# Optimization experiments

Hardware: AMD Instinct MI355X
Metric: run time of the kernel (lower is better)

## Reference

```python
import jax, jax.numpy as jnp
import numpy as np

B, X, Y, Z, T = 2, 32, 32, 32, 16
WIDTH = 20
M1, M2, M3, M4 = 8, 8, 8, 6
N_LAYERS = 8  # octant count per spectral layer


def spectral_conv4d(x, w_ri, m1, m2, m3, m4):
    """x: [B, Ci, X, Y, Z, T] real. w_ri: [8, Ci, Co, m1, m2, m3, m4, 2] real/imag."""
    w = w_ri[..., 0] + 1j * w_ri[..., 1]  # [8, Ci, Co, m1, m2, m3, m4] complex64
    b, ci = x.shape[0], x.shape[1]
    xs, ys, zs, ts = x.shape[2], x.shape[3], x.shape[4], x.shape[5]
    co = w.shape[2]
    # fftn followed by keeping last-dim modes [:m4] equals rfftn at those bins
    x_ft = jnp.fft.rfftn(x, axes=(-4, -3, -2, -1))  # [B, Ci, X, Y, Z, T//2+1]
    out_ft = jnp.zeros((b, co, xs, ys, zs, ts // 2 + 1), dtype=x_ft.dtype)
    idx = 0
    for s1 in (slice(0, m1), slice(xs - m1, xs)):
        for s2 in (slice(0, m2), slice(ys - m2, ys)):
            for s3 in (slice(0, m3), slice(zs - m3, zs)):
                blk = jnp.einsum('bixyzt,ioxyzt->boxyzt',
                                 x_ft[:, :, s1, s2, s3, :m4], w[idx])
                out_ft = out_ft.at[:, :, s1, s2, s3, :m4].set(blk)
                idx += 1
    return jnp.fft.irfftn(out_ft, s=(xs, ys, zs, ts), axes=(-4, -3, -2, -1))


def gelu(x):
    return jax.nn.gelu(x, approximate=False)  # matches torch F.gelu (erf)


def setup_inputs() -> dict:
    key = jax.random.key(0)
    ks = jax.random.split(key, 10)
    scale = 1.0 / (WIDTH * WIDTH)
    return {
        'x': jax.random.normal(ks[0], (B, X, Y, Z, T, 5), dtype=jnp.float32),
        'fc0_w': jax.random.normal(ks[1], (5, WIDTH), dtype=jnp.float32) * 0.3,
        'fc0_b': jax.random.normal(ks[2], (WIDTH,), dtype=jnp.float32) * 0.1,
        'sw': jax.random.uniform(ks[3], (4, 8, WIDTH, WIDTH, M1, M2, M3, M4, 2),
                                 dtype=jnp.float32) * scale,
        'ww': jax.random.normal(ks[4], (4, WIDTH, WIDTH), dtype=jnp.float32) * 0.15,
        'wb': jax.random.normal(ks[5], (4, WIDTH), dtype=jnp.float32) * 0.1,
        'fc1_w': jax.random.normal(ks[6], (WIDTH, 128), dtype=jnp.float32) * 0.15,
        'fc1_b': jax.random.normal(ks[7], (128,), dtype=jnp.float32) * 0.1,
        'fc2_w': jax.random.normal(ks[8], (128, 1), dtype=jnp.float32) * 0.1,
        'fc2_b': jax.random.normal(ks[9], (1,), dtype=jnp.float32) * 0.1,
    }


def reference(x, fc0_w, fc0_b, sw, ww, wb, fc1_w, fc1_b, fc2_w, fc2_b):
    # Lift: [B, X, Y, Z, T, 5] -> [B, X, Y, Z, T, W] -> channels-first
    h = jnp.einsum('bxyzti,iw->bxyztw', x, fc0_w) + fc0_b
    h = jnp.transpose(h, (0, 5, 1, 2, 3, 4))  # [B, W, X, Y, Z, T]
    for l in range(4):
        h1 = spectral_conv4d(h, sw[l], M1, M2, M3, M4)
        h2 = jnp.einsum('bixyzt,oi->boxyzt', h, ww[l]) \
             + wb[l][None, :, None, None, None, None]
        h = h1 + h2
        if l < 3:
            h = gelu(h)  # dropout is identity at inference
    h = jnp.transpose(h, (0, 2, 3, 4, 5, 1))  # [B, X, Y, Z, T, W]
    h = gelu(jnp.einsum('bxyztw,wh->bxyzth', h, fc1_w) + fc1_b)
    out = jnp.einsum('bxyzth,ho->bxyzto', h, fc2_w) + fc2_b
    return out
```

## Files before the change

kernel.cpp:

```cpp
#include <hip/hip_runtime.h>

typedef float2 cplx;

#define SPAT 524288
#define TWO_PI_16 0.39269908169872414f
#define TWO_PI_32 0.19634954084936207f

#define H_OFF   0u
#define A_OFF   83886080u
#define BT_OFF  (83886080u + 31457280u)
#define CT_OFF  (83886080u + 31457280u + 7864320u)
#define FLAG_OFF (83886080u + 31457280u + 7864320u + 7864320u)
#define WS_NEED (FLAG_OFF + 64u)

__device__ __forceinline__ float bf2f(unsigned short s){
    union { unsigned int u; float f; } v; v.u = ((unsigned int)s) << 16; return v.f;
}
__device__ __forceinline__ unsigned short f2bf(float f){
    union { float ff; unsigned int u; } v; v.ff = f;
    unsigned int u = v.u;
    u += 0x7fffu + ((u >> 16) & 1u);
    return (unsigned short)(u >> 16);
}
__device__ __forceinline__ cplx bf2c(unsigned int p){
    union { unsigned int u; float f; } a, b;
    a.u = p << 16; b.u = p & 0xffff0000u;
    cplx r; r.x = a.f; r.y = b.f; return r;
}
__device__ __forceinline__ float LDR(const void* p, size_t i, int bf){
    return bf ? bf2f(((const unsigned short*)p)[i]) : ((const float*)p)[i];
}
__device__ __forceinline__ void STR(void* p, size_t i, float v, int bf){
    if (bf) ((unsigned short*)p)[i] = f2bf(v);
    else    ((float*)p)[i] = v;
}
__device__ __forceinline__ void cmadd(cplx& d, const cplx a, const cplx b){
    d.x = fmaf(a.x, b.x, d.x);
    d.x = fmaf(-a.y, b.y, d.x);
    d.y = fmaf(a.x, b.y, d.y);
    d.y = fmaf(a.y, b.x, d.y);
}
__device__ __forceinline__ int freqm(int m){ return m + ((m >> 3) << 4); }
__device__ __forceinline__ float gelu_f(float v){
    return 0.5f * v * (1.0f + erff(v * 0.7071067811865475f));
}

__global__ void k_detect(const unsigned short* __restrict__ x, int* __restrict__ flag){
    __shared__ int cnts[64];
    const int tid = threadIdx.x;
    int cnt = 0;
    for (int j = tid; j < 512; j += 64){
        unsigned short u = x[2 * j];
        unsigned int e = (u >> 7) & 0xFFu;
        if (e < 27u || e > 160u) cnt++;
    }
    cnts[tid] = cnt;
    __syncthreads();
    if (tid == 0){
        int s = 0;
        for (int i = 0; i < 64; i++) s += cnts[i];
        flag[0] = (s > 64) ? 0 : 1;
    }
}

__global__ __launch_bounds__(256) void k_fc0(const int* __restrict__ flag,
                                             const void* __restrict__ x,
                                             const void* __restrict__ w,
                                             const void* __restrict__ bias,
                                             float* __restrict__ h){
    const int bf = flag[0];
    __shared__ float sw[100];
    __shared__ float sb[20];
    const int tid = threadIdx.x;
    if (tid < 100) sw[tid] = LDR(w, tid, bf);
    if (tid < 20)  sb[tid] = LDR(bias, tid, bf);
    __syncthreads();
    const int p = blockIdx.x * 256 + tid;
    const int b = p >> 19;
    const int rem = p & (SPAT - 1);
    float xi[5];
    #pragma unroll
    for (int i = 0; i < 5; i++) xi[i] = LDR(x, (size_t)p * 5 + i, bf);
    const size_t ob = (size_t)b * 20 * SPAT + rem;
    #pragma unroll
    for (int c = 0; c < 20; c++){
        float acc = sb[c];
        #pragma unroll
        for (int i = 0; i < 5; i++) acc = fmaf(xi[i], sw[i * 20 + c], acc);
        h[ob + (size_t)c * SPAT] = acc;
    }
}

__global__ __launch_bounds__(512, 4) void k_fwdTZY(const float* __restrict__ h, cplx* __restrict__ A2){
    const int x  = blockIdx.x;
    const int bc = blockIdx.y;
    __shared__ __align__(16) float buf[12356];
    __shared__ cplx w16[16];
    __shared__ cplx twZ[16][33];
    const int tid = threadIdx.x;
    if (tid < 16){
        float s, c; sincosf(-TWO_PI_16 * (float)tid, &s, &c);
        w16[tid] = make_float2(c, s);
    }
    if (tid < 512){
        int m = tid >> 5, z = tid & 31;
        float s, c; sincosf(-TWO_PI_32 * (float)((freqm(m) * z) & 31), &s, &c);
        twZ[m][z] = make_float2(c, s);
    }
    __syncthreads();
    cplx wreg[16];
    #pragma unroll
    for (int j = 0; j < 16; j++) wreg[j] = w16[j];
    const float* src = h + ((size_t)bc * 1024 + x * 32) * 512;
    #pragma unroll
    for (int r = 0; r < 2; r++){
        int l = tid + (r << 9);
        int zz = l & 31, y = l >> 5;
        const float4* g = (const float4*)(src + (size_t)y * 512 + zz * 16);
        float4 q0 = g[0], q1 = g[1], q2 = g[2], q3 = g[3];
        float v[16] = {q0.x,q0.y,q0.z,q0.w, q1.x,q1.y,q1.z,q1.w,
                       q2.x,q2.y,q2.z,q2.w, q3.x,q3.y,q3.z,q3.w};
        const int W = y * 386 + zz * 12 + 2 * (zz >> 3);
        float s0 = 0.f;
        #pragma unroll
        for (int t = 0; t < 16; t++) s0 += v[t];
        *(cplx*)&buf[W] = make_float2(s0, 0.f);
        #pragma unroll
        for (int k = 1; k < 6; k++){
            float ax = 0.f, ay = 0.f;
            #pragma unroll
            for (int t = 0; t < 16; t++){
                cplx w = wreg[(k * t) & 15];
                ax = fmaf(v[t], w.x, ax);
                ay = fmaf(v[t], w.y, ay);
            }
            *(cplx*)&buf[W + 2 * k] = make_float2(ax, ay);
        }
    }
    __syncthreads();
    cplx acc2[6];
    #pragma unroll
    for (int r = 0; r < 6; r++){
        int idx = tid + (r << 9);
        int y = idx & 31, q = idx >> 5;
        int k = q % 6, mz = q / 6;
        cplx a = make_float2(0.f, 0.f);
        #pragma unroll
        for (int zz = 0; zz < 32; zz++){
            cplx vz = *(const cplx*)&buf[y * 386 + zz * 12 + 2 * (zz >> 3) + 2 * k];
            cmadd(a, vz, twZ[mz][zz]);
        }
        acc2[r] = a;
    }
    __syncthreads();
    #pragma unroll
    for (int r = 0; r < 6; r++){
        int idx = tid + (r << 9);
        int y = idx & 31, q = idx >> 5;
        *(cplx*)&buf[y * 194 + q * 2] = acc2[r];
    }
    __syncthreads();
    #pragma unroll
    for (int r = 0; r < 3; r++){
        int idx = tid + (r << 9);
        int my = idx & 15, q = idx >> 4;
        int k = q % 6, mz = q / 6;
        cplx a = make_float2(0.f, 0.f);
        #pragma unroll
        for (int y = 0; y < 32; y++){
            cplx vz = *(const cplx*)&buf[y * 194 + q * 2];
            cmadd(a, vz, twZ[my][y]);
        }
        A2[(((size_t)bc * 16 + mz) * 32 + x) * 96 + k * 16 + my] = a;
    }
}

__global__ __launch_bounds__(256) void k_fwdX(const cplx* __restrict__ A2, cplx* __restrict__ Bt){
    const int mz = blockIdx.x;
    const int bc = blockIdx.y;
    __shared__ __align__(16) float inb[32 * 194];
    __shared__ cplx tw[16][33];
    const int tid = threadIdx.x;
    for (int i = tid; i < 512; i += 256){
        int m = i >> 5, p = i & 31;
        float s, c; sincosf(-TWO_PI_32 * (float)((freqm(m) * p) & 31), &s, &c);
        tw[m][p] = make_float2(c, s);
    }
    const cplx* src = A2 + ((size_t)bc * 16 + mz) * 3072;
    for (int i = tid; i < 3072; i += 256){
        int xx = i / 96, qq = i % 96;
        *(cplx*)&inb[xx * 194 + qq * 2] = src[i];
    }
    __syncthreads();
    #pragma unroll
    for (int r = 0; r < 6; r++){
        int idx = tid + (r << 8);
        int my = idx & 15, q2 = idx >> 4;
        int k = q2 % 6, mx = q2 / 6;
        cplx a = make_float2(0.f, 0.f);
        #pragma unroll
        for (int xx = 0; xx < 32; xx++){
            cplx vz = *(const cplx*)&inb[xx * 194 + (k * 16 + my) * 2];
            cmadd(a, vz, tw[mx][xx]);
        }
        Bt[((size_t)bc * 256 + mx * 16 + my) * 96 + mz * 6 + k] = a;
    }
}

__global__ __launch_bounds__(960) void k_mix(const int* __restrict__ flag,
                                             const cplx* __restrict__ Bt,
                                             const void* __restrict__ sw, size_t loff,
                                             cplx* __restrict__ Ct){
    const int bf = flag[0];
    const int j2 = blockIdx.x, j1 = blockIdx.y, oct = blockIdx.z;
    const int xh = oct >> 2, yh = (oct >> 1) & 1, zh = oct & 1;
    const int mx = xh * 8 + j1, my = yh * 8 + j2;
    __shared__ cplx inS[40][48];
    const int tid = threadIdx.x;
    for (int idx = tid; idx < 1920; idx += 960){
        int m = idx % 48, row = idx / 48;
        inS[row][m] = Bt[((size_t)row * 256 + mx * 16 + my) * 96 + zh * 48 + m];
    }
    __syncthreads();
    const int m = tid % 48;
    const int o = tid / 48;
    cplx a0 = make_float2(0.f, 0.f);
    cplx a1 = make_float2(0.f, 0.f);
    const size_t base = loff + ((size_t)(oct * 20) * 20 + o) * 3072
                             + (size_t)(j1 * 8 + j2) * 48 + m;
    if (bf){
        const unsigned int* swp = (const unsigned int*)sw;
        #pragma unroll 5
        for (int i = 0; i < 20; i++){
            cplx w = bf2c(swp[base + (size_t)i * 20 * 3072]);
            cmadd(a0, inS[i][m], w);
            cmadd(a1, inS[20 + i][m], w);
        }
    } else {
        const float2* swp = (const float2*)sw;
        #pragma unroll 5
        for (int i = 0; i < 20; i++){
            cplx w = swp[base + (size_t)i * 20 * 3072];
            cmadd(a0, inS[i][m], w);
            cmadd(a1, inS[20 + i][m], w);
        }
    }
    const float s = 1.0f / 524288.0f;
    a0.x *= s; a0.y *= s;
    a1.x *= s; a1.y *= s;
    Ct[((size_t)o * 256 + mx * 16 + my) * 96 + zh * 48 + m] = a0;
    Ct[((size_t)(20 + o) * 256 + mx * 16 + my) * 96 + zh * 48 + m] = a1;
}

__global__ __launch_bounds__(256) void k_invXY(const cplx* __restrict__ Ct, cplx* __restrict__ D){
    const int kh = blockIdx.x, mz = blockIdx.y, bo = blockIdx.z;
    __shared__ cplx inS[16][16][3];
    __shared__ cplx midY[16][32][3];
    __shared__ cplx tw[16][32];
    const int tid = threadIdx.x;
    for (int i = tid; i < 512; i += 256){
        int m = i >> 5, p = i & 31;
        float s, c; sincosf(TWO_PI_32 * (float)((freqm(m) * p) & 31), &s, &c);
        tw[m][p] = make_float2(c, s);
    }
    for (int i = tid; i < 768; i += 256){
        int k = i % 3, t2 = i / 3;
        int my = t2 & 15, mx = t2 >> 4;
        inS[mx][my][k] = Ct[((size_t)bo * 256 + mx * 16 + my) * 96 + mz * 6 + kh * 3 + k];
    }
    __syncthreads();
    #pragma unroll
    for (int r = 0; r < 6; r++){
        int idx = tid + (r << 8);
        int k = idx % 3, t2 = idx / 3;
        int y = t2 & 31, mx = t2 >> 5;
        cplx acc = make_float2(0.f, 0.f);
        #pragma unroll
        for (int my = 0; my < 16; my++) cmadd(acc, inS[mx][my][k], tw[my][y]);
        midY[mx][y][k] = acc;
    }
    __syncthreads();
    #pragma unroll
    for (int r = 0; r < 4; r++){
        int idx = tid + (r << 8);
        int y = idx & 31, x = idx >> 5;
        cplx a0 = make_float2(0.f, 0.f), a1 = a0, a2 = a0;
        #pragma unroll
        for (int mx = 0; mx < 16; mx++){
            cplx t0 = tw[mx][x];
            cmadd(a0, midY[mx][y][0], t0);
            cmadd(a1, midY[mx][y][1], t0);
            cmadd(a2, midY[mx][y][2], t0);
        }
        size_t base = ((size_t)bo * 1024 + x * 32 + y) * 96 + mz * 6 + kh * 3;
        D[base] = a0; D[base + 1] = a1; D[base + 2] = a2;
    }
}

template<int GELU>
__global__ __launch_bounds__(512, 4) void k_invZT(const int* __restrict__ flag,
                                               const cplx* __restrict__ D, float* __restrict__ h,
                                               const void* __restrict__ ww, size_t woff,
                                               const void* __restrict__ wbv, size_t boff){
    const int bf = flag[0];
    const int y = blockIdx.x, x = blockIdx.y, b = blockIdx.z;
    __shared__ cplx Dsh[20][96];
    __shared__ __align__(16) cplx E[20][32][6];
    __shared__ cplx twz[16][32];
    __shared__ __align__(16) float sww[400];
    __shared__ float swb[20];
    const int tid = threadIdx.x;
    if (tid < 512){
        int m = tid >> 5, z = tid & 31;
        float s, c; sincosf(TWO_PI_32 * (float)((freqm(m) * z) & 31), &s, &c);
        twz[m][z] = make_float2(c, s);
    }
    if (tid < 400) sww[tid] = LDR(ww, woff + tid, bf);
    if (tid < 20)  swb[tid] = LDR(wbv, boff + tid, bf);
    for (int i = tid; i < 1920; i += 512){
        int o = i / 96, m = i % 96;
        Dsh[o][m] = D[((size_t)(b * 20 + o) * 1024 + x * 32 + y) * 96 + m];
    }
    __syncthreads();
    #pragma unroll
    for (int r = 0; r < 8; r++){
        int idx = tid + (r << 9);
        if (idx < 3840){
            int k = idx % 6, t2 = idx / 6;
            int z = t2 & 31, o = t2 >> 5;
            cplx acc = make_float2(0.f, 0.f);
            #pragma unroll
            for (int mz = 0; mz < 16; mz++) cmadd(acc, Dsh[o][mz * 6 + k], twz[mz][z]);
            E[o][z][k] = acc;
        }
    }
    __syncthreads();
    const int t = tid & 15;
    const int z = tid >> 4;
    float ct[6], st[6];
    ct[0] = 1.f; st[0] = 0.f;
    #pragma unroll
    for (int k = 1; k < 6; k++){
        sincosf(TWO_PI_16 * (float)((k * t) & 15), &st[k], &ct[k]);
    }
    const size_t hb = ((size_t)b * 20 * 1024 + x * 32 + y) * 512 + tid;
    float hi[20];
    #pragma unroll
    for (int i = 0; i < 20; i++) hi[i] = h[hb + (size_t)i * SPAT];
    #pragma unroll
    for (int o = 0; o < 20; o++){
        const float4* e = (const float4*)&E[o][z][0];
        float4 a = e[0], bq = e[1], cq = e[2];
        float v = a.x + 2.f * (a.z * ct[1] - a.w * st[1] + bq.x * ct[2] - bq.y * st[2]
                             + bq.z * ct[3] - bq.w * st[3] + cq.x * ct[4] - cq.y * st[4]
                             + cq.z * ct[5] - cq.w * st[5]);
        const float4* wr = (const float4*)&sww[o * 20];
        float4 w0 = wr[0], w1 = wr[1], w2 = wr[2], w3 = wr[3], w4 = wr[4];
        float p = swb[o];
        p = fmaf(hi[ 0], w0.x, p); p = fmaf(hi[ 1], w0.y, p);
        p = fmaf(hi[ 2], w0.z, p); p = fmaf(hi[ 3], w0.w, p);
        p = fmaf(hi[ 4], w1.x, p); p = fmaf(hi[ 5], w1.y, p);
        p = fmaf(hi[ 6], w1.z, p); p = fmaf(hi[ 7], w1.w, p);
        p = fmaf(hi[ 8], w2.x, p); p = fmaf(hi[ 9], w2.y, p);
        p = fmaf(hi[10], w2.z, p); p = fmaf(hi[11], w2.w, p);
        p = fmaf(hi[12], w3.x, p); p = fmaf(hi[13], w3.y, p);
        p = fmaf(hi[14], w3.z, p); p = fmaf(hi[15], w3.w, p);
        p = fmaf(hi[16], w4.x, p); p = fmaf(hi[17], w4.y, p);
        p = fmaf(hi[18], w4.z, p); p = fmaf(hi[19], w4.w, p);
        v += p;
        if (GELU) v = gelu_f(v);
        h[hb + (size_t)o * SPAT] = v;
    }
}

__global__ __launch_bounds__(256) void k_fc12(const int* __restrict__ flag,
                                              const float* __restrict__ h,
                                              const void* __restrict__ w1,
                                              const void* __restrict__ b1,
                                              const void* __restrict__ w2,
                                              const void* __restrict__ b2,
                                              void* __restrict__ out){
    const int bf = flag[0];
    __shared__ __align__(16) float s1[2560];
    __shared__ __align__(16) float sb1[128];
    __shared__ __align__(16) float s2[128];
    const int tid = threadIdx.x;
    for (int i = tid; i < 2560; i += 256) s1[i] = LDR(w1, i, bf);
    if (tid < 128){ sb1[tid] = LDR(b1, tid, bf); s2[tid] = LDR(w2, tid, bf); }
    __syncthreads();
    const int base = blockIdx.x * 256 + tid;
    float hi[4][20];
    #pragma unroll
    for (int q = 0; q < 4; q++){
        int p = base + (q << 18);
        int b = p >> 19, rem = p & (SPAT - 1);
        size_t hbq = (size_t)b * 20 * SPAT + rem;
        #pragma unroll
        for (int i = 0; i < 20; i++) hi[q][i] = h[hbq + (size_t)i * SPAT];
    }
    float acc[4] = {0.f, 0.f, 0.f, 0.f};
    const float fb2 = LDR(b2, 0, bf);
    for (int jc = 0; jc < 32; jc++){
        float4 bb = *(const float4*)&sb1[jc * 4];
        float v[4][4];
        #pragma unroll
        for (int q = 0; q < 4; q++){ v[q][0] = bb.x; v[q][1] = bb.y; v[q][2] = bb.z; v[q][3] = bb.w; }
        #pragma unroll
        for (int i = 0; i < 20; i++){
            float4 w = *(const float4*)&s1[i * 128 + jc * 4];
            #pragma unroll
            for (int q = 0; q < 4; q++){
                v[q][0] = fmaf(hi[q][i], w.x, v[q][0]);
                v[q][1] = fmaf(hi[q][i], w.y, v[q][1]);
                v[q][2] = fmaf(hi[q][i], w.z, v[q][2]);
                v[q][3] = fmaf(hi[q][i], w.w, v[q][3]);
            }
        }
        float4 w2v = *(const float4*)&s2[jc * 4];
        #pragma unroll
        for (int q = 0; q < 4; q++){
            acc[q] = fmaf(gelu_f(v[q][0]), w2v.x, acc[q]);
            acc[q] = fmaf(gelu_f(v[q][1]), w2v.y, acc[q]);
            acc[q] = fmaf(gelu_f(v[q][2]), w2v.z, acc[q]);
            acc[q] = fmaf(gelu_f(v[q][3]), w2v.w, acc[q]);
        }
    }
    #pragma unroll
    for (int q = 0; q < 4; q++) STR(out, base + (q << 18), acc[q] + fb2, bf);
}

extern "C" void kernel_launch(void* const* d_in, const int* in_sizes, int n_in,
                              void* d_out, int out_size, void* d_ws, size_t ws_size,
                              hipStream_t stream) {
    (void)in_sizes; (void)out_size;
    if (n_in < 10) return;
    if (ws_size < (size_t)WS_NEED) return;
    const void* x    = d_in[0];
    const void* fc0w = d_in[1];
    const void* fc0b = d_in[2];
    const void* sw   = d_in[3];
    const void* ww   = d_in[4];
    const void* wb   = d_in[5];
    const void* fc1w = d_in[6];
    const void* fc1b = d_in[7];
    const void* fc2w = d_in[8];
    const void* fc2b = d_in[9];

    char* ws = (char*)d_ws;
    float* h   = (float*)(ws + H_OFF);
    cplx*  A2  = (cplx*)(ws + A_OFF);
    cplx*  Bt  = (cplx*)(ws + BT_OFF);
    cplx*  Ct  = (cplx*)(ws + CT_OFF);
    cplx*  Dd  = (cplx*)(ws + A_OFF);
    int*   flag = (int*)(ws + FLAG_OFF);

    k_detect<<<1, 64, 0, stream>>>((const unsigned short*)x, flag);
    k_fc0<<<4096, 256, 0, stream>>>(flag, x, fc0w, fc0b, h);
    for (int l = 0; l < 4; l++){
        size_t sw_off = (size_t)l * 9830400;
        size_t ww_off = (size_t)l * 400;
        size_t wb_off = (size_t)l * 20;
        k_fwdTZY<<<dim3(32, 40), 512, 0, stream>>>(h, A2);
        k_fwdX<<<dim3(16, 40), 256, 0, stream>>>(A2, Bt);
        k_mix<<<dim3(8, 8, 8), 960, 0, stream>>>(flag, Bt, sw, sw_off, Ct);
        k_invXY<<<dim3(2, 16, 40), 256, 0, stream>>>(Ct, Dd);
        if (l < 3) k_invZT<1><<<dim3(32, 32, 2), 512, 0, stream>>>(flag, Dd, h, ww, ww_off, wb, wb_off);
        else       k_invZT<0><<<dim3(32, 32, 2), 512, 0, stream>>>(flag, Dd, h, ww, ww_off, wb, wb_off);
    }
    k_fc12<<<1024, 256, 0, stream>>>(flag, h, fc1w, fc1b, fc2w, fc2b, d_out);
}
```

Before: 1.353 ms.

## Exploit DFT half-period symmetry in forward and inverse transforms; polynomial erf GELU

Each forward DFT stage (T, Z, Y, X) now first does a butterfly over the two halves of the input, so even and odd frequency bins are computed from 16-point sums/differences instead of full 32- or 16-point sums. The inverse Y/X/Z stages split even and odd frequencies and produce both output halves from one pair of partial sums. This roughly halves the multiply-add count at the cost of extra shared-memory passes and barriers. GELU's erff is replaced by the Abramowitz–Stegun polynomial with a fast reciprocal and exp, which adds approximation error of about 1e-7.

```diff
diff --git a/kernel.cpp b/kernel.cpp
--- a/kernel.cpp
+++ b/kernel.cpp
@@ -42,7 +42,17 @@
 }
 __device__ __forceinline__ int freqm(int m){ return m + ((m >> 3) << 4); }
 __device__ __forceinline__ float gelu_f(float v){
-    return 0.5f * v * (1.0f + erff(v * 0.7071067811865475f));
+    float u = fabsf(v) * 0.7071067811865475f;
+    float t = __builtin_amdgcn_rcpf(fmaf(0.3275911f, u, 1.0f));
+    float p = fmaf(1.061405429f, t, -1.453152027f);
+    p = fmaf(p, t, 1.421413741f);
+    p = fmaf(p, t, -0.284496736f);
+    p = fmaf(p, t, 0.254829592f);
+    p *= t;
+    float e = __expf(-u * u);
+    float g = fmaf(-p, e, 1.0f);
+    g = copysignf(g, v);
+    return 0.5f * v * (1.0f + g);
 }
 
 __global__ void k_detect(const unsigned short* __restrict__ x, int* __restrict__ flag){
@@ -120,22 +130,45 @@
         float4 q0 = g[0], q1 = g[1], q2 = g[2], q3 = g[3];
         float v[16] = {q0.x,q0.y,q0.z,q0.w, q1.x,q1.y,q1.z,q1.w,
                        q2.x,q2.y,q2.z,q2.w, q3.x,q3.y,q3.z,q3.w};
+        float s8[8], d8[8];
+        #pragma unroll
+        for (int t0 = 0; t0 < 8; t0++){ s8[t0] = v[t0] + v[t0 + 8]; d8[t0] = v[t0] - v[t0 + 8]; }
         const int W = y * 386 + zz * 12 + 2 * (zz >> 3);
-        float s0 = 0.f;
-        #pragma unroll
-        for (int t = 0; t < 16; t++) s0 += v[t];
+        float s0 = ((s8[0]+s8[1])+(s8[2]+s8[3]))+((s8[4]+s8[5])+(s8[6]+s8[7]));
         *(cplx*)&buf[W] = make_float2(s0, 0.f);
         #pragma unroll
         for (int k = 1; k < 6; k++){
             float ax = 0.f, ay = 0.f;
-            #pragma unroll
-            for (int t = 0; t < 16; t++){
-                cplx w = wreg[(k * t) & 15];
-                ax = fmaf(v[t], w.x, ax);
-                ay = fmaf(v[t], w.y, ay);
+            if (k & 1){
+                #pragma unroll
+                for (int t0 = 0; t0 < 8; t0++){
+                    cplx w = wreg[(k * t0) & 15];
+                    ax = fmaf(d8[t0], w.x, ax);
+                    ay = fmaf(d8[t0], w.y, ay);
+                }
+            } else {
+                #pragma unroll
+                for (int t0 = 0; t0 < 8; t0++){
+                    cplx w = wreg[(k * t0) & 15];
+                    ax = fmaf(s8[t0], w.x, ax);
+                    ay = fmaf(s8[t0], w.y, ay);
+                }
             }
             *(cplx*)&buf[W + 2 * k] = make_float2(ax, ay);
         }
+    }
+    __syncthreads();
+    #pragma unroll
+    for (int r = 0; r < 6; r++){
+        int idx = tid + (r << 9);
+        int k = idx % 6, t2 = idx / 6;
+        int zz0 = t2 & 15, y = t2 >> 4;
+        int Wa = y * 386 + zz0 * 12 + 2 * (zz0 >> 3) + 2 * k;
+        int zb = zz0 + 16;
+        int Wb = y * 386 + zb * 12 + 2 * (zb >> 3) + 2 * k;
+        cplx a = *(cplx*)&buf[Wa], b = *(cplx*)&buf[Wb];
+        *(cplx*)&buf[Wa] = make_float2(a.x + b.x, a.y + b.y);
+        *(cplx*)&buf[Wb] = make_float2(a.x - b.x, a.y - b.y);
     }
     __syncthreads();
     cplx acc2[6];
@@ -144,11 +177,13 @@
         int idx = tid + (r << 9);
         int y = idx & 31, q = idx >> 5;
         int k = q % 6, mz = q / 6;
+        int off = (mz & 1) << 4;
         cplx a = make_float2(0.f, 0.f);
         #pragma unroll
-        for (int zz = 0; zz < 32; zz++){
+        for (int zz0 = 0; zz0 < 16; zz0++){
+            int zz = zz0 + off;
             cplx vz = *(const cplx*)&buf[y * 386 + zz * 12 + 2 * (zz >> 3) + 2 * k];
-            cmadd(a, vz, twZ[mz][zz]);
+            cmadd(a, vz, twZ[mz][zz0]);
         }
         acc2[r] = a;
     }
@@ -163,13 +198,24 @@
     #pragma unroll
     for (int r = 0; r < 3; r++){
         int idx = tid + (r << 9);
+        int q = idx % 96, y0 = idx / 96;
+        int Wa = y0 * 194 + q * 2, Wb = (y0 + 16) * 194 + q * 2;
+        cplx a = *(cplx*)&buf[Wa], b = *(cplx*)&buf[Wb];
+        *(cplx*)&buf[Wa] = make_float2(a.x + b.x, a.y + b.y);
+        *(cplx*)&buf[Wb] = make_float2(a.x - b.x, a.y - b.y);
+    }
+    __syncthreads();
+    #pragma unroll
+    for (int r = 0; r < 3; r++){
+        int idx = tid + (r << 9);
         int my = idx & 15, q = idx >> 4;
         int k = q % 6, mz = q / 6;
+        int off = (my & 1) << 4;
         cplx a = make_float2(0.f, 0.f);
         #pragma unroll
-        for (int y = 0; y < 32; y++){
-            cplx vz = *(const cplx*)&buf[y * 194 + q * 2];
-            cmadd(a, vz, twZ[my][y]);
+        for (int y0 = 0; y0 < 16; y0++){
+            cplx vz = *(const cplx*)&buf[(y0 + off) * 194 + q * 2];
+            cmadd(a, vz, twZ[my][y0]);
         }
         A2[(((size_t)bc * 16 + mz) * 32 + x) * 96 + k * 16 + my] = a;
     }
@@ -192,16 +238,25 @@
         *(cplx*)&inb[xx * 194 + qq * 2] = src[i];
     }
     __syncthreads();
+    for (int i = tid; i < 1536; i += 256){
+        int xx0 = i / 96, qq = i % 96;
+        int Wa = xx0 * 194 + qq * 2, Wb = (xx0 + 16) * 194 + qq * 2;
+        cplx a = *(cplx*)&inb[Wa], b = *(cplx*)&inb[Wb];
+        *(cplx*)&inb[Wa] = make_float2(a.x + b.x, a.y + b.y);
+        *(cplx*)&inb[Wb] = make_float2(a.x - b.x, a.y - b.y);
+    }
+    __syncthreads();
     #pragma unroll
     for (int r = 0; r < 6; r++){
         int idx = tid + (r << 8);
         int my = idx & 15, q2 = idx >> 4;
         int k = q2 % 6, mx = q2 / 6;
+        int off = (mx & 1) << 4;
         cplx a = make_float2(0.f, 0.f);
         #pragma unroll
-        for (int xx = 0; xx < 32; xx++){
-            cplx vz = *(const cplx*)&inb[xx * 194 + (k * 16 + my) * 2];
-            cmadd(a, vz, tw[mx][xx]);
+        for (int xx0 = 0; xx0 < 16; xx0++){
+            cplx vz = *(const cplx*)&inb[(xx0 + off) * 194 + (k * 16 + my) * 2];
+            cmadd(a, vz, tw[mx][xx0]);
         }
         Bt[((size_t)bc * 256 + mx * 16 + my) * 96 + mz * 6 + k] = a;
     }
@@ -270,30 +325,44 @@
     }
     __syncthreads();
     #pragma unroll
-    for (int r = 0; r < 6; r++){
+    for (int r = 0; r < 3; r++){
         int idx = tid + (r << 8);
         int k = idx % 3, t2 = idx / 3;
-        int y = t2 & 31, mx = t2 >> 5;
-        cplx acc = make_float2(0.f, 0.f);
-        #pragma unroll
-        for (int my = 0; my < 16; my++) cmadd(acc, inS[mx][my][k], tw[my][y]);
-        midY[mx][y][k] = acc;
-    }
-    __syncthreads();
-    #pragma unroll
-    for (int r = 0; r < 4; r++){
+        int y0 = t2 & 15, mx = t2 >> 4;
+        cplx P = make_float2(0.f, 0.f), Q = make_float2(0.f, 0.f);
+        #pragma unroll
+        for (int j = 0; j < 8; j++){
+            cmadd(P, inS[mx][2 * j][k],     tw[2 * j][y0]);
+            cmadd(Q, inS[mx][2 * j + 1][k], tw[2 * j + 1][y0]);
+        }
+        midY[mx][y0][k]      = make_float2(P.x + Q.x, P.y + Q.y);
+        midY[mx][y0 + 16][k] = make_float2(P.x - Q.x, P.y - Q.y);
+    }
+    __syncthreads();
+    #pragma unroll
+    for (int r = 0; r < 2; r++){
         int idx = tid + (r << 8);
-        int y = idx & 31, x = idx >> 5;
-        cplx a0 = make_float2(0.f, 0.f), a1 = a0, a2 = a0;
-        #pragma unroll
-        for (int mx = 0; mx < 16; mx++){
-            cplx t0 = tw[mx][x];
-            cmadd(a0, midY[mx][y][0], t0);
-            cmadd(a1, midY[mx][y][1], t0);
-            cmadd(a2, midY[mx][y][2], t0);
-        }
-        size_t base = ((size_t)bo * 1024 + x * 32 + y) * 96 + mz * 6 + kh * 3;
-        D[base] = a0; D[base + 1] = a1; D[base + 2] = a2;
+        int y = idx & 31, x0 = idx >> 5;
+        cplx P0 = make_float2(0.f,0.f), P1 = P0, P2 = P0, Q0 = P0, Q1 = P0, Q2 = P0;
+        #pragma unroll
+        for (int j = 0; j < 8; j++){
+            cplx te = tw[2 * j][x0];
+            cmadd(P0, midY[2 * j][y][0], te);
+            cmadd(P1, midY[2 * j][y][1], te);
+            cmadd(P2, midY[2 * j][y][2], te);
+            cplx to = tw[2 * j + 1][x0];
+            cmadd(Q0, midY[2 * j + 1][y][0], to);
+            cmadd(Q1, midY[2 * j + 1][y][1], to);
+            cmadd(Q2, midY[2 * j + 1][y][2], to);
+        }
+        size_t b0 = ((size_t)bo * 1024 + x0 * 32 + y) * 96 + mz * 6 + kh * 3;
+        size_t b1 = ((size_t)bo * 1024 + (x0 + 16) * 32 + y) * 96 + mz * 6 + kh * 3;
+        D[b0]     = make_float2(P0.x + Q0.x, P0.y + Q0.y);
+        D[b0 + 1] = make_float2(P1.x + Q1.x, P1.y + Q1.y);
+        D[b0 + 2] = make_float2(P2.x + Q2.x, P2.y + Q2.y);
+        D[b1]     = make_float2(P0.x - Q0.x, P0.y - Q0.y);
+        D[b1 + 1] = make_float2(P1.x - Q1.x, P1.y - Q1.y);
+        D[b1 + 2] = make_float2(P2.x - Q2.x, P2.y - Q2.y);
     }
 }
 
@@ -323,15 +392,19 @@
     }
     __syncthreads();
     #pragma unroll
-    for (int r = 0; r < 8; r++){
+    for (int r = 0; r < 4; r++){
         int idx = tid + (r << 9);
-        if (idx < 3840){
+        if (idx < 1920){
             int k = idx % 6, t2 = idx / 6;
-            int z = t2 & 31, o = t2 >> 5;
-            cplx acc = make_float2(0.f, 0.f);
+            int z0 = t2 & 15, o = t2 >> 4;
+            cplx P = make_float2(0.f, 0.f), Q = make_float2(0.f, 0.f);
             #pragma unroll
-            for (int mz = 0; mz < 16; mz++) cmadd(acc, Dsh[o][mz * 6 + k], twz[mz][z]);
-            E[o][z][k] = acc;
+            for (int j = 0; j < 8; j++){
+                cmadd(P, Dsh[o][(2 * j) * 6 + k],     twz[2 * j][z0]);
+                cmadd(Q, Dsh[o][(2 * j + 1) * 6 + k], twz[2 * j + 1][z0]);
+            }
+            E[o][z0][k]      = make_float2(P.x + Q.x, P.y + Q.y);
+            E[o][z0 + 16][k] = make_float2(P.x - Q.x, P.y - Q.y);
         }
     }
     __syncthreads();
```

Result: faster. 1.147 ms (-15.2%).
